# Optimization experiments

Measured on AMD Instinct MI355X. Metric: run time of the kernel, lower is better.

Reference implementation:

```python
import jax, jax.numpy as jnp
import numpy as np
from jax import lax

HEADS = 6      # n_splits // head_ratio
DHEAD = 64     # hidden // n_splits
ALLH = HEADS * DHEAD  # 384
KS = 9         # conv_kernel_size
PAD = (KS - 1) // 2


def setup_inputs() -> dict:
    key = jax.random.key(0)
    ks = jax.random.split(key, 12)
    B, S, H = 8, 1024, 768
    f = jnp.float32
    return {
        "Q": jax.random.normal(ks[0], (B, S, H), f),
        "K": jax.random.normal(ks[1], (B, S, H), f),
        "V": jax.random.normal(ks[2], (B, S, H), f),
        "Wq": jax.random.normal(ks[3], (H, ALLH), f) * 0.02,
        "Wk": jax.random.normal(ks[4], (H, ALLH), f) * 0.02,
        "Wv": jax.random.normal(ks[5], (H, ALLH), f) * 0.02,
        "dw": jax.random.normal(ks[6], (H, KS), f) * 0.02,        # depthwise conv [C,k]
        "pw": jax.random.normal(ks[7], (ALLH, H), f) * 0.02,      # pointwise conv [out,in]
        "sep_bias": jnp.zeros((ALLH,), f),
        "Wck": jax.random.normal(ks[8], (ALLH, HEADS * KS), f) * 0.02,
        "bck": jnp.zeros((HEADS * KS,), f),
        "Wco": jax.random.normal(ks[9], (H, ALLH), f) * 0.02,
        "bco": jnp.zeros((ALLH,), f),
        "gammas": jnp.zeros((HEADS, 1, 1), f),
        "mask": jnp.ones((B, S), jnp.int32),
    }


def _forward(Q, K, V, Wq, Wk, Wv, dw, pw, sep_bias, Wck, bck, Wco, bco, gammas, mask):
    B, S, H = Q.shape
    q = Q @ Wq  # [B,S,ALLH]
    k = K @ Wk
    v = V @ Wv
    # SeparableConv1D on K: depthwise 'same' conv (groups=H) then 1x1 pointwise + bias
    x = K.transpose(0, 2, 1)  # [B,H,S]
    x = lax.conv_general_dilated(x, dw[:, None, :], (1,), [(PAD, PAD)],
                                 dimension_numbers=("NCH", "OIH", "NCH"),
                                 feature_group_count=H)
    keyconv = jnp.einsum("bcs,oc->bso", x, pw) + sep_bias  # [B,S,ALLH]
    # span-dynamic-conv kernel weights, softmax over kernel taps
    conv_attn = keyconv * q
    kern = (conv_attn @ Wck + bck).reshape(B, S, HEADS, KS)
    kern = jax.nn.softmax(kern, axis=-1)
    # unfold V-projection into local windows and apply per-position kernels
    co = V @ Wco + bco                                   # [B,S,ALLH]
    cop = jnp.pad(co, ((0, 0), (PAD, PAD), (0, 0)))
    win = jnp.stack([cop[:, j:j + S, :] for j in range(KS)], axis=-1)  # [B,S,ALLH,KS]
    win = win.reshape(B, S, HEADS, DHEAD, KS)
    conv_out = jnp.einsum("bshdk,bshk->bshd", win, kern)  # [B,S,HEADS,DHEAD]
    # standard attention scores
    q4 = q.reshape(B, S, HEADS, DHEAD).transpose(0, 2, 1, 3)
    k4 = k.reshape(B, S, HEADS, DHEAD).transpose(0, 2, 1, 3)
    v4 = v.reshape(B, S, HEADS, DHEAD).transpose(0, 2, 1, 3)
    scores = jnp.einsum("bhid,bhjd->bhij", q4, k4) / jnp.sqrt(jnp.float32(DHEAD))
    m = (mask != 0)[:, None, None, :]  # key mask [B,1,1,S]
    # monotonic distance scores (no-grad in original -> stop_gradient)
    sc = lax.stop_gradient(scores)
    p_ = jax.nn.softmax(jnp.where(m, sc, -1e32), axis=-1) * m.astype(sc.dtype)
    cum = jnp.cumsum(p_, axis=-1)
    tot = jnp.sum(p_, axis=-1, keepdims=True)
    idx = jnp.arange(S)
    pos = jnp.abs(idx[None, :] - idx[:, None]).astype(jnp.float32)  # |i-j|
    dist = jnp.sqrt(jnp.clip((tot - cum) * pos, 0.0))
    gamma = -jax.nn.softplus(gammas)[None]  # [1,HEADS,1,1]
    effect = jnp.clip(jnp.exp(dist * gamma), 1e-5, 1e5)
    scores2 = jnp.where(m, scores * effect, -1e8)
    probs = jax.nn.softmax(scores2, axis=-1)  # dropout_p=0 -> identity
    ctx = jnp.einsum("bhij,bhjd->bihd", probs, v4)  # [B,S,HEADS,DHEAD]
    out = jnp.concatenate([ctx, conv_out], axis=2).reshape(B, S, 2 * ALLH)
    return out


def reference(Q, K, V, Wq, Wk, Wv, dw, pw, sep_bias, Wck, bck, Wco, bco, gammas, mask):
    return _forward(Q, K, V, Wq, Wk, Wv, dw, pw, sep_bias, Wck, bck, Wco, bco, gammas, mask)
```

## Files before the change

kernel.cpp:

```cpp
#include <hip/hip_runtime.h>
#include <math.h>

#define BATCH 8
#define SEQ   1024
#define HID   768
#define HEADS 6
#define DHEAD 64
#define ALLH  384
#define KS    9
#define PADC  4
#define MROWS (BATCH*SEQ)

typedef __attribute__((ext_vector_type(8))) short bf16x8;
typedef __attribute__((ext_vector_type(4))) short bf16x4;
typedef __attribute__((ext_vector_type(4))) float f32x4;

__device__ __forceinline__ ushort f2bf(float x) {
    unsigned u = __float_as_uint(x);
    unsigned r = (u + 0x7FFFu + ((u >> 16) & 1u)) >> 16;
    return (ushort)r;
}
__device__ __forceinline__ unsigned pk2(float a, float b) {
    return (unsigned)f2bf(a) | ((unsigned)f2bf(b) << 16);
}
__device__ __forceinline__ float fexp2(float x) {
#if __has_builtin(__builtin_amdgcn_exp2f)
    return __builtin_amdgcn_exp2f(x);
#else
    return exp2f(x);
#endif
}
__device__ __forceinline__ float fsqrt(float x) {
#if __has_builtin(__builtin_amdgcn_sqrtf)
    return __builtin_amdgcn_sqrtf(x);
#else
    return __sqrtf(x);
#endif
}
__device__ __forceinline__ unsigned cvtpk(float a, float b) {
    unsigned r; asm("v_cvt_pk_bf16_f32 %0, %1, %2" : "=v"(r) : "v"(a), "v"(b)); return r;
}

__device__ __forceinline__ void mfma16(f32x4& c4, bf16x4 a, bf16x4 b) {
#if __has_builtin(__builtin_amdgcn_mfma_f32_16x16x16bf16_1k)
    c4 = __builtin_amdgcn_mfma_f32_16x16x16bf16_1k(a, b, c4, 0, 0, 0);
#else
    asm volatile("v_mfma_f32_16x16x16_bf16 %0, %1, %2, %0" : "+v"(c4) : "v"(a), "v"(b));
#endif
}

__global__ __launch_bounds__(256) void dconv_kernel(const float* __restrict__ Kin,
                                                    const float* __restrict__ dw,
                                                    ushort* __restrict__ y) {
    const int t = threadIdx.x;
    const int c4l = t & 63;
    const int sg = t >> 6;
    const int c4 = blockIdx.x * 64 + c4l;
    const int s0 = blockIdx.y * 64 + sg * 16;
    const int b = blockIdx.z;
    const int c = c4 * 4;

    const float* base = Kin + (size_t)b * SEQ * HID + c;
    ushort* ybase = y + (size_t)b * SEQ * HID + c;

    float wv[4][KS];
#pragma unroll
    for (int j = 0; j < 4; ++j)
#pragma unroll
        for (int tt = 0; tt < KS; ++tt) wv[j][tt] = dw[(c + j) * KS + tt];

    float4 win[KS];
#pragma unroll
    for (int tt = 0; tt < KS; ++tt) {
        int sj = s0 - PADC + tt;
        win[tt] = (sj >= 0 && sj < SEQ) ? *reinterpret_cast<const float4*>(base + (size_t)sj * HID)
                                        : float4{0.f, 0.f, 0.f, 0.f};
    }

#pragma unroll
    for (int i = 0; i < 16; ++i) {
        const int s = s0 + i;
        float4 acc = {0.f, 0.f, 0.f, 0.f};
#pragma unroll
        for (int tt = 0; tt < KS; ++tt) {
            acc.x += win[tt].x * wv[0][tt];
            acc.y += win[tt].y * wv[1][tt];
            acc.z += win[tt].z * wv[2][tt];
            acc.w += win[tt].w * wv[3][tt];
        }
        uint2 o;
        o.x = pk2(acc.x, acc.y); o.y = pk2(acc.z, acc.w);
        *reinterpret_cast<uint2*>(ybase + (size_t)s * HID) = o;
#pragma unroll
        for (int tt = 0; tt < KS - 1; ++tt) win[tt] = win[tt + 1];
        int sj = s + 1 + PADC;
        win[KS - 1] = (sj < SEQ) ? *reinterpret_cast<const float4*>(base + (size_t)sj * HID)
                                 : float4{0.f, 0.f, 0.f, 0.f};
    }
}

__global__ __launch_bounds__(256) void wcvt_kernel(const float* __restrict__ W0, const float* __restrict__ W1,
                                                   const float* __restrict__ W2, const float* __restrict__ W3,
                                                   ushort* __restrict__ O0, ushort* __restrict__ O1,
                                                   ushort* __restrict__ O2, ushort* __restrict__ O3) {
    __shared__ float t[32][33];
    int wsel = blockIdx.z;
    const float* W = wsel == 0 ? W0 : wsel == 1 ? W1 : wsel == 2 ? W2 : W3;
    ushort* O = wsel == 0 ? O0 : wsel == 1 ? O1 : wsel == 2 ? O2 : O3;
    int kt = blockIdx.x * 32;
    int nt = blockIdx.y * 32;
    int tx = threadIdx.x & 31, ty = threadIdx.x >> 5;
#pragma unroll
    for (int i = 0; i < 4; ++i)
        t[ty + i * 8][tx] = W[(size_t)(kt + ty + i * 8) * ALLH + nt + tx];
    __syncthreads();
#pragma unroll
    for (int i = 0; i < 4; ++i)
        O[(size_t)(nt + ty + i * 8) * HID + kt + tx] = f2bf(t[tx][ty + i * 8]);
}

__global__ __launch_bounds__(256) void pwcvt_kernel(const float* __restrict__ pw, ushort* __restrict__ pwb) {
    int i = blockIdx.x * 256 + threadIdx.x;
    if (i < ALLH * HID) pwb[i] = f2bf(pw[i]);
}

__global__ __launch_bounds__(256) void gemm_all(const float* __restrict__ Q,
                                                const float* __restrict__ Kin,
                                                const float* __restrict__ V,
                                                const ushort* __restrict__ ybf,
                                                const ushort* __restrict__ WqT,
                                                const ushort* __restrict__ WkT,
                                                const ushort* __restrict__ WvT,
                                                const ushort* __restrict__ WcoT,
                                                const ushort* __restrict__ pwT,
                                                const float* __restrict__ bco,
                                                const float* __restrict__ sep_bias,
                                                float* __restrict__ qb,
                                                ushort* __restrict__ qh,
                                                ushort* __restrict__ khm,
                                                ushort* __restrict__ vhm,
                                                float* __restrict__ cob,
                                                float* __restrict__ kcb) {
    __shared__ __align__(16) ushort As[128 * 64];
    __shared__ __align__(16) ushort Bs[128 * 64];

    const int bx = blockIdx.x;
    const int swz = (bx & 7) * 120 + (bx >> 3);
    const int unit = swz / 192;
    const int local = swz % 192;
    const int n0 = (local % 3) * 128;
    const int m0 = (local / 3) * 128;

    const float* Af = unit == 0 ? Q : unit == 1 ? Kin : V;
    const ushort* Ab = ybf;
    const ushort* Bt = unit == 0 ? WqT : unit == 1 ? WkT : unit == 2 ? WvT : unit == 3 ? WcoT : pwT;
    const bool af32 = (unit != 4);

    const int tid = threadIdx.x;
    const int lane = tid & 63;
    const int w = tid >> 6;
    const int wr = w >> 1, wc = w & 1;
    const int g = lane >> 4;
    const int c = lane & 15;

    f32x4 acc[4][4];
#pragma unroll
    for (int i = 0; i < 4; ++i)
#pragma unroll
        for (int j = 0; j < 4; ++j) acc[i][j] = f32x4{0.f, 0.f, 0.f, 0.f};

    for (int k0 = 0; k0 < HID; k0 += 64) {
        __syncthreads();
#pragma unroll
        for (int it = 0; it < 4; ++it) {
            int e = tid + it * 256;
            int row = e >> 3;
            int c8 = (e & 7) * 8;
            int boff = row * 128 + ((c8 * 2) ^ ((row & 7) << 4));
            if (af32) {
                const float4 f0 = *reinterpret_cast<const float4*>(&Af[(size_t)(m0 + row) * HID + k0 + c8]);
                const float4 f1 = *reinterpret_cast<const float4*>(&Af[(size_t)(m0 + row) * HID + k0 + c8 + 4]);
                uint4 p;
                p.x = pk2(f0.x, f0.y); p.y = pk2(f0.z, f0.w);
                p.z = pk2(f1.x, f1.y); p.w = pk2(f1.z, f1.w);
                *reinterpret_cast<uint4*>((char*)As + boff) = p;
            } else {
                const uint4 av = *reinterpret_cast<const uint4*>(&Ab[(size_t)(m0 + row) * HID + k0 + c8]);
                *reinterpret_cast<uint4*>((char*)As + boff) = av;
            }
            const uint4 bv = *reinterpret_cast<const uint4*>(&Bt[(size_t)(n0 + row) * HID + k0 + c8]);
            *reinterpret_cast<uint4*>((char*)Bs + boff) = bv;
        }
        __syncthreads();

        bf16x8 af0[4], af1[4];
#pragma unroll
        for (int mq = 0; mq < 4; ++mq) {
            const int arow = wr * 64 + mq * 16 + c;
            const int asw = (arow & 7) << 4;
            af0[mq] = *reinterpret_cast<const bf16x8*>((char*)As + arow * 128 + ((g * 16) ^ asw));
            af1[mq] = *reinterpret_cast<const bf16x8*>((char*)As + arow * 128 + ((64 + g * 16) ^ asw));
        }
#pragma unroll
        for (int nq = 0; nq < 4; ++nq) {
            const int brow = wc * 64 + nq * 16 + c;
            const int bsw = (brow & 7) << 4;
            bf16x8 bf0 = *reinterpret_cast<const bf16x8*>((char*)Bs + brow * 128 + ((g * 16) ^ bsw));
            bf16x8 bf1 = *reinterpret_cast<const bf16x8*>((char*)Bs + brow * 128 + ((64 + g * 16) ^ bsw));
#pragma unroll
            for (int mq = 0; mq < 4; ++mq) {
                acc[mq][nq] = __builtin_amdgcn_mfma_f32_16x16x32_bf16(af0[mq], bf0, acc[mq][nq], 0, 0, 0);
                acc[mq][nq] = __builtin_amdgcn_mfma_f32_16x16x32_bf16(af1[mq], bf1, acc[mq][nq], 0, 0, 0);
            }
        }
    }

    if (unit == 2) {
#pragma unroll
        for (int mq = 0; mq < 4; ++mq) {
            const int mbase = m0 + wr * 64 + mq * 16 + g * 4;
            const int bb = mbase >> 10;
            const int st = (mbase & 1023) >> 6;
            const unsigned colb = (unsigned)(32 * mq + 8 * g);
#pragma unroll
            for (int nq = 0; nq < 4; ++nq) {
                const int n = n0 + wc * 64 + nq * 16 + c;
                const int head = n >> 6;
                const int d = n & 63;
                char* tb = (char*)vhm + (((size_t)(bb * HEADS + head) * 16 + st) * 4096) * 2;
                unsigned off = (unsigned)d * 128 + (colb ^ ((d & 7) << 4));
                uint2 vv;
                vv.x = pk2(acc[mq][nq][0], acc[mq][nq][1]);
                vv.y = pk2(acc[mq][nq][2], acc[mq][nq][3]);
                *reinterpret_cast<uint2*>(tb + off) = vv;
            }
        }
        return;
    }

#pragma unroll
    for (int nq = 0; nq < 4; ++nq) {
        const int n = n0 + wc * 64 + nq * 16 + c;
        float bv = 0.f;
        if (unit == 3) bv = bco[n];
        if (unit == 4) bv = sep_bias[n];
#pragma unroll
        for (int mq = 0; mq < 4; ++mq) {
#pragma unroll
            for (int r = 0; r < 4; ++r) {
                const int m = m0 + wr * 64 + mq * 16 + g * 4 + r;
                float v = acc[mq][nq][r] + bv;
                if (unit == 0) {
                    qb[(size_t)m * ALLH + n] = v;
                    int bb = m >> 10, s = m & 1023;
                    int head = n >> 6, d = n & 63;
                    qh[(((size_t)bb * HEADS + head) * SEQ + s) * 64 + d] = f2bf(v);
                } else if (unit == 1) {
                    int bb = m >> 10, s = m & 1023;
                    int head = n >> 6, d = n & 63;
                    char* tb = (char*)khm + (((size_t)(bb * HEADS + head) * 16 + (s >> 6)) * 4096) * 2;
                    unsigned off = (unsigned)(s & 63) * 128 + (((unsigned)(d * 2)) ^ ((s & 7) << 4));
                    *reinterpret_cast<ushort*>(tb + off) = f2bf(v);
                } else if (unit == 3) {
                    cob[(size_t)m * ALLH + n] = v;
                } else {
                    kcb[(size_t)m * ALLH + n] = v;
                }
            }
        }
    }
}

__global__ __launch_bounds__(256) void spankern_kernel(const float* __restrict__ keyconv,
                                                       const float* __restrict__ q,
                                                       const float* __restrict__ Wck,
                                                       const float* __restrict__ bck,
                                                       float* __restrict__ kern_sm) {
    __shared__ float ca[4][ALLH];
    __shared__ float kv[4][64];
    int row0 = blockIdx.x * 4;
    int tid = threadIdx.x;
    int r = tid >> 6;
    int lane = tid & 63;
    int row = row0 + r;
    for (int e = lane; e < ALLH; e += 64) {
        size_t off = (size_t)row * ALLH + e;
        ca[r][e] = keyconv[off] * q[off];
    }
    __syncthreads();
    float val = 0.f;
    if (lane < HEADS * KS) {
        for (int kidx = 0; kidx < ALLH; ++kidx)
            val += ca[r][kidx] * Wck[kidx * (HEADS * KS) + lane];
        val += bck[lane];
    }
    kv[r][lane] = val;
    __syncthreads();
    if (lane < HEADS) {
        float mx = -INFINITY;
#pragma unroll
        for (int t = 0; t < KS; ++t) mx = fmaxf(mx, kv[r][lane * KS + t]);
        float e[KS];
        float sum = 0.f;
#pragma unroll
        for (int t = 0; t < KS; ++t) {
            e[t] = expf(kv[r][lane * KS + t] - mx);
            sum += e[t];
        }
        float inv = 1.f / sum;
#pragma unroll
        for (int t = 0; t < KS; ++t)
            kern_sm[((size_t)row * HEADS + lane) * KS + t] = e[t] * inv;
    }
}

__global__ __launch_bounds__(256) void convout_kernel(const float* __restrict__ co,
                                                      const float* __restrict__ kern_sm,
                                                      float* __restrict__ out) {
    int idx = blockIdx.x * 256 + threadIdx.x;
    if (idx >= MROWS * (ALLH / 4)) return;
    int c4 = idx % (ALLH / 4);
    int s = (idx / (ALLH / 4)) % SEQ;
    int b = idx / ((ALLH / 4) * SEQ);
    int c = c4 * 4;
    int h = c >> 6;
    const float* ks = &kern_sm[(((size_t)b * SEQ + s) * HEADS + h) * KS];
    float kt[KS];
#pragma unroll
    for (int t = 0; t < KS; ++t) kt[t] = ks[t];
    float4 acc = {0.f, 0.f, 0.f, 0.f};
#pragma unroll
    for (int t = 0; t < KS; ++t) {
        int sj = s + t - PADC;
        if (sj >= 0 && sj < SEQ) {
            const float4 cv = *reinterpret_cast<const float4*>(&co[((size_t)b * SEQ + sj) * ALLH + c]);
            acc.x += cv.x * kt[t];
            acc.y += cv.y * kt[t];
            acc.z += cv.z * kt[t];
            acc.w += cv.w * kt[t];
        }
    }
    *reinterpret_cast<float4*>(&out[((size_t)b * SEQ + s) * (2 * ALLH) + ALLH + c]) = acc;
}

__global__ __launch_bounds__(256) void attn_mfma(const ushort* __restrict__ qh,
                                                 const ushort* __restrict__ kh,
                                                 const ushort* __restrict__ vh,
                                                 const int* __restrict__ mask,
                                                 const float* __restrict__ gammas,
                                                 float* __restrict__ out) {
    __shared__ __align__(16) ushort kbuf[64 * 64];
    __shared__ __align__(16) ushort vbuf[64 * 64];
    __shared__ float s_msk[SEQ];

    const int bid = blockIdx.x;
    const int blk = (bid & 7) * 96 + (bid >> 3);
    const int qt = blk & 15;
    const int h = (blk >> 4) % HEADS;
    const int b = blk / (16 * HEADS);
    const int i0 = qt * 64;
    const int tid = threadIdx.x;
    const int lane = tid & 63;
    const int w = tid >> 6;
    const int g = lane >> 4;
    const int c = lane & 15;

    const float LOG2E = 1.44269504f;
    float g0 = gammas[h];
    float gamma2 = -(fmaxf(g0, 0.f) + log1pf(expf(-fabsf(g0)))) * LOG2E;
    const float SLOG2 = 0.125f * LOG2E;

    const ushort* ktiles = kh + ((size_t)(b * HEADS + h) * 16) * 4096;
    const ushort* vtiles = vh + ((size_t)(b * HEADS + h) * 16) * 4096;
    const ushort* qhb = qh + ((size_t)b * HEADS + h) * SEQ * 64;

    for (int e = tid; e < SEQ; e += 256)
        s_msk[e] = (mask[b * SEQ + e] != 0) ? 1.f : 0.f;

    bf16x8 qf0, qf1;
    {
        const ushort* qrow = qhb + (size_t)(i0 + w * 16 + c) * 64 + g * 8;
        qf0 = *reinterpret_cast<const bf16x8*>(qrow);
        qf1 = *reinterpret_cast<const bf16x8*>(qrow + 32);
    }

    float Tacc = 0.f;
    for (int chk = 0; chk < 16; ++chk) {
        __syncthreads();
        const ushort* ktp = ktiles + chk * 4096;
#pragma unroll
        for (int it = 0; it < 2; ++it) {
            int e16 = (tid + it * 256) * 16;
            *reinterpret_cast<uint4*>((char*)kbuf + e16) =
                *reinterpret_cast<const uint4*>((const char*)ktp + e16);
        }
        __syncthreads();
        const int j0 = chk * 64;
#pragma unroll
        for (int m = 0; m < 4; ++m) {
            f32x4 acc = {0.f, 0.f, 0.f, 0.f};
            int row = m * 16 + c;
            int sw = (row & 7) << 4;
            bf16x8 kf0 = *reinterpret_cast<const bf16x8*>((char*)kbuf + row * 128 + ((g * 16) ^ sw));
            bf16x8 kf1 = *reinterpret_cast<const bf16x8*>((char*)kbuf + row * 128 + ((64 + g * 16) ^ sw));
            acc = __builtin_amdgcn_mfma_f32_16x16x32_bf16(kf0, qf0, acc, 0, 0, 0);
            acc = __builtin_amdgcn_mfma_f32_16x16x32_bf16(kf1, qf1, acc, 0, 0, 0);
#pragma unroll
            for (int r = 0; r < 4; ++r) {
                float mk = s_msk[j0 + m * 16 + g * 4 + r];
                Tacc += mk * fexp2(acc[r] * SLOG2);
            }
        }
    }
    Tacc += __shfl_xor(Tacc, 16, 64);
    Tacc += __shfl_xor(Tacc, 32, 64);
    const float T = Tacc;
    const float invT = (T > 0.f) ? 1.f / T : 0.f;

    f32x4 ctx0 = {0,0,0,0}, ctx1 = {0,0,0,0}, ctx2 = {0,0,0,0}, ctx3 = {0,0,0,0};
    float l2acc = 0.f;
    float base = 0.f;
    const float iq = (float)(i0 + w * 16 + c);
    const unsigned vx = (unsigned)((c & 7) << 4);

    for (int chk = 0; chk < 16; ++chk) {
        __syncthreads();
        const ushort* ktp = ktiles + chk * 4096;
        const ushort* vtp = vtiles + chk * 4096;
#pragma unroll
        for (int it = 0; it < 2; ++it) {
            int e16 = (tid + it * 256) * 16;
            *reinterpret_cast<uint4*>((char*)kbuf + e16) =
                *reinterpret_cast<const uint4*>((const char*)ktp + e16);
            *reinterpret_cast<uint4*>((char*)vbuf + e16) =
                *reinterpret_cast<const uint4*>((const char*)vtp + e16);
        }
        __syncthreads();
        const int j0 = chk * 64;
#pragma unroll
        for (int m = 0; m < 4; ++m) {
            f32x4 acc = {0.f, 0.f, 0.f, 0.f};
            int row = m * 16 + c;
            int sw = (row & 7) << 4;
            bf16x8 kf0 = *reinterpret_cast<const bf16x8*>((char*)kbuf + row * 128 + ((g * 16) ^ sw));
            bf16x8 kf1 = *reinterpret_cast<const bf16x8*>((char*)kbuf + row * 128 + ((64 + g * 16) ^ sw));
            acc = __builtin_amdgcn_mfma_f32_16x16x32_bf16(kf0, qf0, acc, 0, 0, 0);
            acc = __builtin_amdgcn_mfma_f32_16x16x32_bf16(kf1, qf1, acc, 0, 0, 0);

            float sl[4], mk[4], incl[4];
            float li = 0.f;
#pragma unroll
            for (int r = 0; r < 4; ++r) {
                mk[r] = s_msk[j0 + m * 16 + g * 4 + r];
                sl[r] = acc[r] * SLOG2;
                float e = mk[r] * fexp2(sl[r]);
                li += e;
                incl[r] = li;
            }
            float gs = li;
            float up = __shfl_up(gs, 16, 64); if (g >= 1) gs += up;
            up = __shfl_up(gs, 32, 64); if (g >= 2) gs += up;
            float gexcl = gs - li;
            float ttot = __shfl(gs, 48 + c, 64);

            const float dbase = iq - (float)(j0 + m * 16 + g * 4);
            float p2[4];
#pragma unroll
            for (int r = 0; r < 4; ++r) {
                float cum = base + gexcl + incl[r];
                float rem = fmaxf(1.0f - cum * invT, 0.f);
                float pos = fabsf(dbase - (float)r);
                float dist = fsqrt(rem * pos);
                float eff = fmaxf(fexp2(dist * gamma2), 1e-5f);
                p2[r] = mk[r] * fexp2(sl[r] * eff);
                l2acc += p2[r];
            }
            base += ttot;

            union { uint2 u; bf16x4 v; } pu;
            pu.u.x = cvtpk(p2[0], p2[1]);
            pu.u.y = cvtpk(p2[2], p2[3]);
            bf16x4 pa = pu.v;

            const unsigned cb = ((unsigned)(32 * m + 8 * g)) ^ vx;
#pragma unroll
            for (int t = 0; t < 4; ++t) {
                bf16x4 vfrag = *reinterpret_cast<const bf16x4*>((char*)vbuf + (unsigned)(c + 16 * t) * 128 + cb);
                if (t == 0) mfma16(ctx0, pa, vfrag);
                else if (t == 1) mfma16(ctx1, pa, vfrag);
                else if (t == 2) mfma16(ctx2, pa, vfrag);
                else mfma16(ctx3, pa, vfrag);
            }
        }
    }
    l2acc += __shfl_xor(l2acc, 16, 64);
    l2acc += __shfl_xor(l2acc, 32, 64);
    const float invl2 = 1.f / l2acc;

#pragma unroll
    for (int r = 0; r < 4; ++r) {
        float inv_r = __shfl(invl2, g * 4 + r, 64);
        int qrow = i0 + w * 16 + g * 4 + r;
        float* orow = out + ((size_t)b * SEQ + qrow) * (2 * ALLH) + h * DHEAD;
        orow[c +  0] = ctx0[r] * inv_r;
        orow[c + 16] = ctx1[r] * inv_r;
        orow[c + 32] = ctx2[r] * inv_r;
        orow[c + 48] = ctx3[r] * inv_r;
    }
}

extern "C" void kernel_launch(void* const* d_in, const int* in_sizes, int n_in,
                              void* d_out, int out_size, void* d_ws, size_t ws_size,
                              hipStream_t stream) {
    const float* Q = (const float*)d_in[0];
    const float* Kin = (const float*)d_in[1];
    const float* V = (const float*)d_in[2];
    const float* Wq = (const float*)d_in[3];
    const float* Wk = (const float*)d_in[4];
    const float* Wv = (const float*)d_in[5];
    const float* dw = (const float*)d_in[6];
    const float* pw = (const float*)d_in[7];
    const float* sep_bias = (const float*)d_in[8];
    const float* Wck = (const float*)d_in[9];
    const float* bck = (const float*)d_in[10];
    const float* Wco = (const float*)d_in[11];
    const float* bco = (const float*)d_in[12];
    const float* gammas = (const float*)d_in[13];
    const int* mask = (const int*)d_in[14];
    float* out = (float*)d_out;
    float* ws = (float*)d_ws;

    const size_t NP = (size_t)MROWS * ALLH;
    const size_t WSZ = (size_t)ALLH * HID;
    float* qb   = ws;
    float* cob  = qb + NP;
    float* kcb  = cob + NP;
    float* kern = kcb + NP;
    ushort* qh  = (ushort*)(kern + (size_t)MROWS * HEADS * KS);
    ushort* khm = qh + NP;
    ushort* vhm = khm + NP;
    ushort* ybf = vhm + NP;
    ushort* WqT = ybf + (size_t)MROWS * HID;
    ushort* WkT = WqT + WSZ;
    ushort* WvT = WkT + WSZ;
    ushort* WcoT = WvT + WSZ;
    ushort* pwT = WcoT + WSZ;

    dconv_kernel<<<dim3(3, 16, BATCH), 256, 0, stream>>>(Kin, dw, ybf);
    wcvt_kernel<<<dim3(24, 12, 4), 256, 0, stream>>>(Wq, Wk, Wv, Wco, WqT, WkT, WvT, WcoT);
    pwcvt_kernel<<<(ALLH * HID + 255) / 256, 256, 0, stream>>>(pw, pwT);

    gemm_all<<<960, 256, 0, stream>>>(Q, Kin, V, ybf, WqT, WkT, WvT, WcoT, pwT,
                                      bco, sep_bias, qb, qh, khm, vhm, cob, kcb);

    spankern_kernel<<<MROWS / 4, 256, 0, stream>>>(kcb, qb, Wck, bck, kern);

    convout_kernel<<<(MROWS * (ALLH / 4) + 255) / 256, 256, 0, stream>>>(cob, kern, out);

    attn_mfma<<<BATCH * HEADS * (SEQ / 64), 256, 0, stream>>>(qh, khm, vhm, mask, gammas, out);
}
```

Baseline: 226.4 us.

## Shrink fused GEMM tiles to 64x64 and prefetch next K-slice into registers

The fused projection GEMM now uses 64x64 output tiles (3840 blocks instead of 960), with each wave owning a 16-row strip across all 64 columns. Global loads for the next K-slice are issued into registers before the current slice's MFMAs run, a register double-buffer meant to hide memory latency. The smaller tiles raise occupancy and parallelism but lower reuse, so A and B are re-read from global memory more often. The V-head epilogue is simplified because each tile now maps to a single head and seq block.

```diff
diff --git a/kernel.cpp b/kernel.cpp
--- a/kernel.cpp
+++ b/kernel.cpp
@@ -141,15 +141,15 @@
                                                 ushort* __restrict__ vhm,
                                                 float* __restrict__ cob,
                                                 float* __restrict__ kcb) {
-    __shared__ __align__(16) ushort As[128 * 64];
-    __shared__ __align__(16) ushort Bs[128 * 64];
+    __shared__ __align__(16) ushort As[64 * 64];
+    __shared__ __align__(16) ushort Bs[64 * 64];
 
     const int bx = blockIdx.x;
-    const int swz = (bx & 7) * 120 + (bx >> 3);
-    const int unit = swz / 192;
-    const int local = swz % 192;
-    const int n0 = (local % 3) * 128;
-    const int m0 = (local / 3) * 128;
+    const int swz = (bx & 7) * 480 + (bx >> 3);
+    const int unit = swz / 768;
+    const int local = swz % 768;
+    const int n0 = (local % 6) * 64;
+    const int m0 = (local / 6) * 64;
 
     const float* Af = unit == 0 ? Q : unit == 1 ? Kin : V;
     const ushort* Ab = ybf;
@@ -159,113 +159,111 @@
     const int tid = threadIdx.x;
     const int lane = tid & 63;
     const int w = tid >> 6;
-    const int wr = w >> 1, wc = w & 1;
     const int g = lane >> 4;
     const int c = lane & 15;
 
-    f32x4 acc[4][4];
-#pragma unroll
-    for (int i = 0; i < 4; ++i)
-#pragma unroll
-        for (int j = 0; j < 4; ++j) acc[i][j] = f32x4{0.f, 0.f, 0.f, 0.f};
-
-    for (int k0 = 0; k0 < HID; k0 += 64) {
+    const int r0 = tid >> 3;
+    const int r1 = r0 + 32;
+    const int c8 = (tid & 7) * 8;
+    const int b0 = r0 * 128 + ((c8 * 2) ^ ((r0 & 7) << 4));
+    const int b1 = r1 * 128 + ((c8 * 2) ^ ((r1 & 7) << 4));
+
+    uint4 ar0, ar1, br0, br1;
+    float4 f0a, f0b, f1a, f1b;
+    auto loadAB = [&](int k0) {
+        if (af32) {
+            f0a = *reinterpret_cast<const float4*>(&Af[(size_t)(m0 + r0) * HID + k0 + c8]);
+            f0b = *reinterpret_cast<const float4*>(&Af[(size_t)(m0 + r0) * HID + k0 + c8 + 4]);
+            f1a = *reinterpret_cast<const float4*>(&Af[(size_t)(m0 + r1) * HID + k0 + c8]);
+            f1b = *reinterpret_cast<const float4*>(&Af[(size_t)(m0 + r1) * HID + k0 + c8 + 4]);
+        } else {
+            ar0 = *reinterpret_cast<const uint4*>(&Ab[(size_t)(m0 + r0) * HID + k0 + c8]);
+            ar1 = *reinterpret_cast<const uint4*>(&Ab[(size_t)(m0 + r1) * HID + k0 + c8]);
+        }
+        br0 = *reinterpret_cast<const uint4*>(&Bt[(size_t)(n0 + r0) * HID + k0 + c8]);
+        br1 = *reinterpret_cast<const uint4*>(&Bt[(size_t)(n0 + r1) * HID + k0 + c8]);
+    };
+    loadAB(0);
+
+    f32x4 acc[4] = {{0,0,0,0},{0,0,0,0},{0,0,0,0},{0,0,0,0}};
+
+    const int arow = w * 16 + c;
+    const int asw = (arow & 7) << 4;
+
+    for (int ks = 0; ks < 12; ++ks) {
         __syncthreads();
-#pragma unroll
-        for (int it = 0; it < 4; ++it) {
-            int e = tid + it * 256;
-            int row = e >> 3;
-            int c8 = (e & 7) * 8;
-            int boff = row * 128 + ((c8 * 2) ^ ((row & 7) << 4));
-            if (af32) {
-                const float4 f0 = *reinterpret_cast<const float4*>(&Af[(size_t)(m0 + row) * HID + k0 + c8]);
-                const float4 f1 = *reinterpret_cast<const float4*>(&Af[(size_t)(m0 + row) * HID + k0 + c8 + 4]);
-                uint4 p;
-                p.x = pk2(f0.x, f0.y); p.y = pk2(f0.z, f0.w);
-                p.z = pk2(f1.x, f1.y); p.w = pk2(f1.z, f1.w);
-                *reinterpret_cast<uint4*>((char*)As + boff) = p;
-            } else {
-                const uint4 av = *reinterpret_cast<const uint4*>(&Ab[(size_t)(m0 + row) * HID + k0 + c8]);
-                *reinterpret_cast<uint4*>((char*)As + boff) = av;
-            }
-            const uint4 bv = *reinterpret_cast<const uint4*>(&Bt[(size_t)(n0 + row) * HID + k0 + c8]);
-            *reinterpret_cast<uint4*>((char*)Bs + boff) = bv;
-        }
+        if (af32) {
+            uint4 p0, p1;
+            p0.x = pk2(f0a.x, f0a.y); p0.y = pk2(f0a.z, f0a.w);
+            p0.z = pk2(f0b.x, f0b.y); p0.w = pk2(f0b.z, f0b.w);
+            p1.x = pk2(f1a.x, f1a.y); p1.y = pk2(f1a.z, f1a.w);
+            p1.z = pk2(f1b.x, f1b.y); p1.w = pk2(f1b.z, f1b.w);
+            *reinterpret_cast<uint4*>((char*)As + b0) = p0;
+            *reinterpret_cast<uint4*>((char*)As + b1) = p1;
+        } else {
+            *reinterpret_cast<uint4*>((char*)As + b0) = ar0;
+            *reinterpret_cast<uint4*>((char*)As + b1) = ar1;
+        }
+        *reinterpret_cast<uint4*>((char*)Bs + b0) = br0;
+        *reinterpret_cast<uint4*>((char*)Bs + b1) = br1;
         __syncthreads();
-
-        bf16x8 af0[4], af1[4];
-#pragma unroll
-        for (int mq = 0; mq < 4; ++mq) {
-            const int arow = wr * 64 + mq * 16 + c;
-            const int asw = (arow & 7) << 4;
-            af0[mq] = *reinterpret_cast<const bf16x8*>((char*)As + arow * 128 + ((g * 16) ^ asw));
-            af1[mq] = *reinterpret_cast<const bf16x8*>((char*)As + arow * 128 + ((64 + g * 16) ^ asw));
-        }
+        if (ks < 11) loadAB((ks + 1) * 64);
+
+        bf16x8 af0 = *reinterpret_cast<const bf16x8*>((char*)As + arow * 128 + ((g * 16) ^ asw));
+        bf16x8 af1 = *reinterpret_cast<const bf16x8*>((char*)As + arow * 128 + ((64 + g * 16) ^ asw));
 #pragma unroll
         for (int nq = 0; nq < 4; ++nq) {
-            const int brow = wc * 64 + nq * 16 + c;
+            const int brow = nq * 16 + c;
             const int bsw = (brow & 7) << 4;
             bf16x8 bf0 = *reinterpret_cast<const bf16x8*>((char*)Bs + brow * 128 + ((g * 16) ^ bsw));
             bf16x8 bf1 = *reinterpret_cast<const bf16x8*>((char*)Bs + brow * 128 + ((64 + g * 16) ^ bsw));
-#pragma unroll
-            for (int mq = 0; mq < 4; ++mq) {
-                acc[mq][nq] = __builtin_amdgcn_mfma_f32_16x16x32_bf16(af0[mq], bf0, acc[mq][nq], 0, 0, 0);
-                acc[mq][nq] = __builtin_amdgcn_mfma_f32_16x16x32_bf16(af1[mq], bf1, acc[mq][nq], 0, 0, 0);
-            }
+            acc[nq] = __builtin_amdgcn_mfma_f32_16x16x32_bf16(af0, bf0, acc[nq], 0, 0, 0);
+            acc[nq] = __builtin_amdgcn_mfma_f32_16x16x32_bf16(af1, bf1, acc[nq], 0, 0, 0);
         }
     }
 
     if (unit == 2) {
-#pragma unroll
-        for (int mq = 0; mq < 4; ++mq) {
-            const int mbase = m0 + wr * 64 + mq * 16 + g * 4;
-            const int bb = mbase >> 10;
-            const int st = (mbase & 1023) >> 6;
-            const unsigned colb = (unsigned)(32 * mq + 8 * g);
-#pragma unroll
-            for (int nq = 0; nq < 4; ++nq) {
-                const int n = n0 + wc * 64 + nq * 16 + c;
-                const int head = n >> 6;
-                const int d = n & 63;
-                char* tb = (char*)vhm + (((size_t)(bb * HEADS + head) * 16 + st) * 4096) * 2;
-                unsigned off = (unsigned)d * 128 + (colb ^ ((d & 7) << 4));
-                uint2 vv;
-                vv.x = pk2(acc[mq][nq][0], acc[mq][nq][1]);
-                vv.y = pk2(acc[mq][nq][2], acc[mq][nq][3]);
-                *reinterpret_cast<uint2*>(tb + off) = vv;
-            }
+        const int head = n0 >> 6;
+        const int bb = m0 >> 10;
+        const int st = (m0 & 1023) >> 6;
+        char* tb = (char*)vhm + (((size_t)(bb * HEADS + head) * 16 + st) * 4096) * 2;
+#pragma unroll
+        for (int nq = 0; nq < 4; ++nq) {
+            const int d = nq * 16 + c;
+            unsigned off = (unsigned)d * 128 + (((unsigned)(32 * w + 8 * g)) ^ ((d & 7) << 4));
+            uint2 vv;
+            vv.x = pk2(acc[nq][0], acc[nq][1]);
+            vv.y = pk2(acc[nq][2], acc[nq][3]);
+            *reinterpret_cast<uint2*>(tb + off) = vv;
         }
         return;
     }
 
 #pragma unroll
     for (int nq = 0; nq < 4; ++nq) {
-        const int n = n0 + wc * 64 + nq * 16 + c;
+        const int n = n0 + nq * 16 + c;
         float bv = 0.f;
         if (unit == 3) bv = bco[n];
         if (unit == 4) bv = sep_bias[n];
 #pragma unroll
-        for (int mq = 0; mq < 4; ++mq) {
-#pragma unroll
-            for (int r = 0; r < 4; ++r) {
-                const int m = m0 + wr * 64 + mq * 16 + g * 4 + r;
-                float v = acc[mq][nq][r] + bv;
-                if (unit == 0) {
-                    qb[(size_t)m * ALLH + n] = v;
-                    int bb = m >> 10, s = m & 1023;
-                    int head = n >> 6, d = n & 63;
-                    qh[(((size_t)bb * HEADS + head) * SEQ + s) * 64 + d] = f2bf(v);
-                } else if (unit == 1) {
-                    int bb = m >> 10, s = m & 1023;
-                    int head = n >> 6, d = n & 63;
-                    char* tb = (char*)khm + (((size_t)(bb * HEADS + head) * 16 + (s >> 6)) * 4096) * 2;
-                    unsigned off = (unsigned)(s & 63) * 128 + (((unsigned)(d * 2)) ^ ((s & 7) << 4));
-                    *reinterpret_cast<ushort*>(tb + off) = f2bf(v);
-                } else if (unit == 3) {
-                    cob[(size_t)m * ALLH + n] = v;
-                } else {
-                    kcb[(size_t)m * ALLH + n] = v;
-                }
+        for (int r = 0; r < 4; ++r) {
+            const int m = m0 + w * 16 + g * 4 + r;
+            float v = acc[nq][r] + bv;
+            if (unit == 0) {
+                qb[(size_t)m * ALLH + n] = v;
+                int bb = m >> 10, s = m & 1023;
+                int head = n >> 6, d = n & 63;
+                qh[(((size_t)bb * HEADS + head) * SEQ + s) * 64 + d] = f2bf(v);
+            } else if (unit == 1) {
+                int bb = m >> 10, s = m & 1023;
+                int head = n >> 6, d = n & 63;
+                char* tb = (char*)khm + (((size_t)(bb * HEADS + head) * 16 + (s >> 6)) * 4096) * 2;
+                unsigned off = (unsigned)(s & 63) * 128 + (((unsigned)(d * 2)) ^ ((s & 7) << 4));
+                *reinterpret_cast<ushort*>(tb + off) = f2bf(v);
+            } else if (unit == 3) {
+                cob[(size_t)m * ALLH + n] = v;
+            } else {
+                kcb[(size_t)m * ALLH + n] = v;
             }
         }
     }
@@ -550,8 +548,8 @@
     wcvt_kernel<<<dim3(24, 12, 4), 256, 0, stream>>>(Wq, Wk, Wv, Wco, WqT, WkT, WvT, WcoT);
     pwcvt_kernel<<<(ALLH * HID + 255) / 256, 256, 0, stream>>>(pw, pwT);
 
-    gemm_all<<<960, 256, 0, stream>>>(Q, Kin, V, ybf, WqT, WkT, WvT, WcoT, pwT,
-                                      bco, sep_bias, qb, qh, khm, vhm, cob, kcb);
+    gemm_all<<<3840, 256, 0, stream>>>(Q, Kin, V, ybf, WqT, WkT, WvT, WcoT, pwT,
+                                       bco, sep_bias, qb, qh, khm, vhm, cob, kcb);
 
     spankern_kernel<<<MROWS / 4, 256, 0, stream>>>(kcb, qb, Wck, bck, kern);
 
```

Measured after the change: 228.9 us. No clear change (+1.1%).
